# Kernel optimization log

Measured on AMD Instinct MI355X. Metric: run time of the kernel, lower is better.

The kernel has to match this reference:

```python
import jax, jax.numpy as jnp
import numpy as np
from jax import lax

K = 3
STRIDE = 1
PAD = 1
DIL = 1


def setup_inputs() -> dict:
    key = jax.random.key(0)
    k1, k2, k3 = jax.random.split(key, 3)
    B, C, H, W = 8, 128, 64, 64
    O = 128
    x = jax.random.normal(k1, (B, C, H, W), jnp.float32)
    # offset-predicting conv weights (small init -> small offsets, as in DCN practice)
    w_off = jax.random.normal(k2, (2 * K * K, C, K, K), jnp.float32) * 0.01
    b_off = jnp.zeros((2 * K * K,), jnp.float32)
    # deformable conv weight [O, Cin, K, K], bias=False in the source
    w = jax.random.normal(k3, (O, C, K, K), jnp.float32) * (1.0 / np.sqrt(C * K * K))
    return {"x": x, "w_off": w_off, "b_off": b_off, "w": w}


def _deform_conv(x, offset, w):
    # x: [B,C,H,W]; offset: [B, 2*K*K, Ho, Wo]; w: [O,C,K,K]
    B, C, H, W = x.shape
    Ho, Wo = offset.shape[2], offset.shape[3]
    K2 = K * K
    off = offset.reshape(B, K2, 2, Ho, Wo)
    oy, ox = off[:, :, 0], off[:, :, 1]            # [B,K2,Ho,Wo]
    ky = (jnp.arange(K2) // K).astype(jnp.float32)  # kernel row per tap
    kx = (jnp.arange(K2) % K).astype(jnp.float32)
    base_y = (jnp.arange(Ho) * STRIDE - PAD).astype(jnp.float32)
    base_x = (jnp.arange(Wo) * STRIDE - PAD).astype(jnp.float32)
    py = base_y[None, None, :, None] + ky[None, :, None, None] * DIL + oy
    px = base_x[None, None, None, :] + kx[None, :, None, None] * DIL + ox

    y0 = jnp.floor(py)
    x0 = jnp.floor(px)
    dy = py - y0
    dx = px - x0
    y0i = y0.astype(jnp.int32)
    x0i = x0.astype(jnp.int32)
    bidx = jnp.arange(B)[:, None, None, None]

    def gather(yi, xi):
        valid = (yi >= 0) & (yi < H) & (xi >= 0) & (xi < W)
        yc = jnp.clip(yi, 0, H - 1)
        xc = jnp.clip(xi, 0, W - 1)
        v = x[bidx, :, yc, xc]  # [B,K2,Ho,Wo,C]
        return v * valid[..., None]

    v00 = gather(y0i, x0i)
    v01 = gather(y0i, x0i + 1)
    v10 = gather(y0i + 1, x0i)
    v11 = gather(y0i + 1, x0i + 1)
    samp = (v00 * ((1 - dy) * (1 - dx))[..., None]
            + v01 * ((1 - dy) * dx)[..., None]
            + v10 * (dy * (1 - dx))[..., None]
            + v11 * (dy * dx)[..., None])  # [B,K2,Ho,Wo,C]

    O = w.shape[0]
    return jnp.einsum('bkhwc,ock->bohw', samp, w.reshape(O, C, K2))


def reference(x, w_off, b_off, w):
    # offset conv: standard conv2d, stride/pad/dilation as in __init__
    offset = lax.conv_general_dilated(
        x, w_off, window_strides=(STRIDE, STRIDE),
        padding=[(PAD, PAD), (PAD, PAD)], rhs_dilation=(DIL, DIL))
    offset = offset + b_off[None, :, None, None]
    return _deform_conv(x, offset, w)
```

## Files before the change

### kernel.cpp

```cpp
#include <hip/hip_runtime.h>

#define B_ 8
#define C_ 128
#define H_ 64
#define W_ 64
#define O_ 128
#define F_ 18
#define K2_ 9
#define HW_ 4096
#define CK2_ 1152

typedef __attribute__((ext_vector_type(8))) short short8_t;
typedef __attribute__((ext_vector_type(4))) float f32x4_t;

__device__ inline short bf16r(float f) {
  unsigned u = __builtin_bit_cast(unsigned, f);
  u += 0x7FFFu + ((u >> 16) & 1u);
  return (short)(u >> 16);
}
__device__ inline float bf2f(short s) {
  unsigned u = ((unsigned)(unsigned short)s) << 16;
  return __builtin_bit_cast(float, u);
}

__global__ __launch_bounds__(256) void prep_all_kernel(
    const float* __restrict__ w, const float* __restrict__ w_off,
    const float* __restrict__ x,
    short* __restrict__ w_bt2, short* __restrict__ w_ot2,
    short* __restrict__ x_t) {
  __shared__ float tile[128][65];
  int bid = blockIdx.x, t = threadIdx.x;
  if (bid < 576) {
    int i = bid * 256 + t;
    int kk2 = i & 31, o = (i >> 5) & 127, ks = i >> 12;
    w_bt2[i] = bf16r(w[(o * C_ + (ks & 3) * 32 + kk2) * K2_ + (ks >> 2)]);
  } else if (bid < 720) {
    int i = (bid - 576) * 256 + t;
    int kk2 = i & 31, f = (i >> 5) & 31, ks = i >> 10;
    w_ot2[i] = (f < F_) ? bf16r(w_off[(f * C_ + (ks & 3) * 32 + kk2) * K2_ + (ks >> 2)])
                        : (short)0;
  } else {
    int xb_id = bid - 720;
    int b = xb_id >> 6;
    int p_base = (xb_id & 63) << 6;
    const float* xb = x + ((long)b << 19);
#pragma unroll
    for (int i = 0; i < 32; ++i) {
      int idx = (i << 8) + t;
      int c = idx >> 6, p = idx & 63;
      tile[c][p] = xb[((long)c << 12) + p_base + p];
    }
    __syncthreads();
#pragma unroll
    for (int i = 0; i < 32; ++i) {
      int idx = (i << 8) + t;
      int p = idx >> 7, c = idx & 127;
      x_t[(((long)(b << 12) + p_base + p) << 7) + c] = bf16r(tile[c][p]);
    }
  }
}

__device__ inline short8_t lds16(const short* xs, int pix, int ch) {
  return *(const short8_t*)(xs + (pix << 7) + ((ch ^ (pix & 7)) << 3));
}

__global__ __launch_bounds__(512, 2) void fused_deform_kernel(
    const short* __restrict__ x_t, const short* __restrict__ w_ot2,
    const float* __restrict__ b_off, const short* __restrict__ w_bt2,
    float* __restrict__ out) {
  __shared__ short xs[8 * 64 * 128];

  int tid = threadIdx.x;
  int wv = tid >> 6, lane = tid & 63;
  int fr = lane & 15, q = lane >> 4;
  int bid = (int)blockIdx.x;
  int b = bid & 7;
  int strip = bid >> 3;
  int ho0 = strip << 1;
  int ys = max(ho0 - 3, 0), ye = min(ho0 + 4, H_ - 1);

  const short* xtb = x_t + ((long)b << 19);

#pragma unroll
  for (int i = 0; i < 16; ++i) {
    int ci = (i << 9) + tid;
    int pix = ci >> 4, ch = ci & 15;
    int y = ys + (pix >> 6);
    if (y <= ye) {
      short8_t v = *(const short8_t*)(xtb + (((y << 6) + (pix & 63)) << 7) + (ch << 3));
      *(short8_t*)(xs + (pix << 7) + ((ch ^ (pix & 7)) << 3)) = v;
    }
  }
  __syncthreads();

  int pos_l = (wv << 4) + fr;
  int row_l = pos_l >> 6;
  int wo = pos_l & 63;
  int ho = ho0 + row_l;

  f32x4_t oacc0 = (f32x4_t){0.f, 0.f, 0.f, 0.f};
  f32x4_t oacc1 = (f32x4_t){0.f, 0.f, 0.f, 0.f};
#pragma unroll
  for (int kt = 0; kt < 9; ++kt) {
    int y = ho + kt / 3 - 1, xx = wo + kt % 3 - 1;
    bool ok = (y >= 0) & (y < H_) & (xx >= 0) & (xx < W_);
    int yc = min(max(y, 0), H_ - 1), xc = min(max(xx, 0), W_ - 1);
    int pixA = ((yc - ys) << 6) + xc;
#pragma unroll
    for (int s = 0; s < 4; ++s) {
      short8_t bfv = lds16(xs, pixA, (s << 2) + q);
      if (!ok) bfv = (short8_t){0, 0, 0, 0, 0, 0, 0, 0};
      int ks = (kt << 2) + s;
      short8_t a0 = *(const short8_t*)(w_ot2 + (((ks << 5) + fr) << 5) + (q << 3));
      short8_t a1 = *(const short8_t*)(w_ot2 + (((ks << 5) + 16 + fr) << 5) + (q << 3));
      oacc0 = __builtin_amdgcn_mfma_f32_16x16x32_bf16(a0, bfv, oacc0, 0, 0, 0);
      oacc1 = __builtin_amdgcn_mfma_f32_16x16x32_bf16(a1, bfv, oacc1, 0, 0, 0);
    }
  }

  f32x4_t acc[8];
#pragma unroll
  for (int nf = 0; nf < 8; ++nf) acc[nf] = (f32x4_t){0.f, 0.f, 0.f, 0.f};

#pragma unroll
  for (int kt = 0; kt < 9; ++kt) {
    float oy, ox;
    if (kt < 8) {
      oy = __shfl(oacc0[(2 * kt) & 3], fr + ((kt >> 1) << 4), 64);
      ox = __shfl(oacc0[(2 * kt + 1) & 3], fr + ((kt >> 1) << 4), 64);
    } else {
      oy = __shfl(oacc1[0], fr, 64);
      ox = __shfl(oacc1[1], fr, 64);
    }
    oy += b_off[2 * kt];
    ox += b_off[2 * kt + 1];

    float py = (float)(ho + kt / 3 - 1) + oy;
    float px = (float)(wo + kt % 3 - 1) + ox;
    float fy0 = floorf(py), fx0 = floorf(px);
    float dy = py - fy0, dx = px - fx0;
    int y0 = (int)fy0, x0 = (int)fx0;
    int y1 = y0 + 1, x1 = x0 + 1;
    float my0 = (y0 >= 0 && y0 < H_) ? 1.f : 0.f;
    float my1 = (y1 >= 0 && y1 < H_) ? 1.f : 0.f;
    float mx0 = (x0 >= 0 && x0 < W_) ? 1.f : 0.f;
    float mx1 = (x1 >= 0 && x1 < W_) ? 1.f : 0.f;
    float w00 = (1.f - dy) * (1.f - dx) * my0 * mx0;
    float w01 = (1.f - dy) * dx * my0 * mx1;
    float w10 = dy * (1.f - dx) * my1 * mx0;
    float w11 = dy * dx * my1 * mx1;
    int y0c = min(max(y0, 0), H_ - 1), y1c = min(max(y1, 0), H_ - 1);
    int x0c = min(max(x0, 0), W_ - 1), x1c = min(max(x1, 0), W_ - 1);
    int p00 = ((y0c - ys) << 6) + x0c, p01 = ((y0c - ys) << 6) + x1c;
    int p10 = ((y1c - ys) << 6) + x0c, p11 = ((y1c - ys) << 6) + x1c;

    short8_t v00[4], v01[4], v10[4], v11[4];
    unsigned long long bad = __ballot((y0c < ys) || (y1c > ye));
    if (bad == 0ULL) {
#pragma unroll
      for (int s = 0; s < 4; ++s) {
        int ch = (s << 2) + q;
        v00[s] = lds16(xs, p00, ch);
        v01[s] = lds16(xs, p01, ch);
        v10[s] = lds16(xs, p10, ch);
        v11[s] = lds16(xs, p11, ch);
      }
    } else {
      const short* g00 = xtb + (((y0c << 6) + x0c) << 7);
      const short* g01 = xtb + (((y0c << 6) + x1c) << 7);
      const short* g10 = xtb + (((y1c << 6) + x0c) << 7);
      const short* g11 = xtb + (((y1c << 6) + x1c) << 7);
#pragma unroll
      for (int s = 0; s < 4; ++s) {
        int c0 = (s << 5) + (q << 3);
        v00[s] = *(const short8_t*)(g00 + c0);
        v01[s] = *(const short8_t*)(g01 + c0);
        v10[s] = *(const short8_t*)(g10 + c0);
        v11[s] = *(const short8_t*)(g11 + c0);
      }
    }

#pragma unroll
    for (int s = 0; s < 4; ++s) {
      short8_t sf;
#pragma unroll
      for (int j = 0; j < 8; ++j) {
        float v = w00 * bf2f(v00[s][j]) + w01 * bf2f(v01[s][j]) +
                  w10 * bf2f(v10[s][j]) + w11 * bf2f(v11[s][j]);
        sf[j] = bf16r(v);
      }
      int ks = (kt << 2) + s;
      const short* wp = w_bt2 + (((ks << 7) + fr) << 5) + (q << 3);
#pragma unroll
      for (int nf = 0; nf < 8; ++nf) {
        short8_t wf = *(const short8_t*)(wp + (nf << 9));
        acc[nf] = __builtin_amdgcn_mfma_f32_16x16x32_bf16(wf, sf, acc[nf], 0, 0, 0);
      }
    }
  }

  float* ob = out + ((long)(b * O_) << 12) + (ho << 6) + wo;
#pragma unroll
  for (int nf = 0; nf < 8; ++nf) {
#pragma unroll
    for (int r = 0; r < 4; ++r) {
      ob[(long)(((nf << 4) + (q << 2) + r)) << 12] = acc[nf][r];
    }
  }
}

extern "C" void kernel_launch(void* const* d_in, const int* in_sizes, int n_in,
                              void* d_out, int out_size, void* d_ws, size_t ws_size,
                              hipStream_t stream) {
  const float* x     = (const float*)d_in[0];
  const float* w_off = (const float*)d_in[1];
  const float* b_off = (const float*)d_in[2];
  const float* w     = (const float*)d_in[3];
  float* out = (float*)d_out;

  short* w_bt2 = (short*)d_ws;
  short* w_ot2 = (short*)((char*)d_ws + 294912);
  short* x_t   = (short*)((char*)d_ws + 294912 + 73728);

  prep_all_kernel<<<1232, 256, 0, stream>>>(w, w_off, x, w_bt2, w_ot2, x_t);
  fused_deform_kernel<<<256, 512, 0, stream>>>(x_t, w_ot2, b_off, w_bt2, out);
}
```

Before: 61.90 us.

## Use 2D 8x16 output tiles with smaller LDS halo and packed bf16 conversion

Changes each block's work from a two-row full-width strip to an 8x16 2D tile. This shrinks the staged LDS halo window to 14x22 pixels, which allows four blocks per CU instead of two. It also replaces the per-element bf16 unpack and round with 32-bit lo/hi extraction and the hardware v_cvt_pk_bf16_f32 instruction. The extra x-direction halo bound check may send more waves to the global-memory fallback path, and the bf16 rounding now depends on the hardware converter rather than the software round.

```diff
diff --git a/kernel.cpp b/kernel.cpp
--- a/kernel.cpp
+++ b/kernel.cpp
@@ -10,17 +10,23 @@
 #define HW_ 4096
 #define CK2_ 1152
 
+#define WR_ 14
+#define WC_ 22
+
 typedef __attribute__((ext_vector_type(8))) short short8_t;
 typedef __attribute__((ext_vector_type(4))) float f32x4_t;
+typedef __attribute__((ext_vector_type(4))) unsigned int uint4_t;
 
 __device__ inline short bf16r(float f) {
   unsigned u = __builtin_bit_cast(unsigned, f);
   u += 0x7FFFu + ((u >> 16) & 1u);
   return (short)(u >> 16);
 }
-__device__ inline float bf2f(short s) {
-  unsigned u = ((unsigned)(unsigned short)s) << 16;
-  return __builtin_bit_cast(float, u);
+__device__ inline float bflo(unsigned u) {
+  return __builtin_bit_cast(float, u << 16);
+}
+__device__ inline float bfhi(unsigned u) {
+  return __builtin_bit_cast(float, u & 0xFFFF0000u);
 }
 
 __global__ __launch_bounds__(256) void prep_all_kernel(
@@ -64,39 +70,40 @@
   return *(const short8_t*)(xs + (pix << 7) + ((ch ^ (pix & 7)) << 3));
 }
 
-__global__ __launch_bounds__(512, 2) void fused_deform_kernel(
+__global__ __launch_bounds__(512, 4) void fused_deform_kernel(
     const short* __restrict__ x_t, const short* __restrict__ w_ot2,
     const float* __restrict__ b_off, const short* __restrict__ w_bt2,
     float* __restrict__ out) {
-  __shared__ short xs[8 * 64 * 128];
+  __shared__ short xs[WR_ * WC_ * 128];
 
   int tid = threadIdx.x;
   int wv = tid >> 6, lane = tid & 63;
   int fr = lane & 15, q = lane >> 4;
   int bid = (int)blockIdx.x;
   int b = bid & 7;
-  int strip = bid >> 3;
-  int ho0 = strip << 1;
-  int ys = max(ho0 - 3, 0), ye = min(ho0 + 4, H_ - 1);
+  int tile_id = bid >> 3;
+  int ho0 = (tile_id >> 2) << 3;
+  int x0b = (tile_id & 3) << 4;
+  int ys  = min(max(ho0 - 3, 0), H_ - WR_);
+  int xsL = min(max(x0b - 3, 0), W_ - WC_);
+  int ye2 = ys + WR_ - 1, xe2 = xsL + WC_ - 1;
 
   const short* xtb = x_t + ((long)b << 19);
 
 #pragma unroll
-  for (int i = 0; i < 16; ++i) {
+  for (int i = 0; i < 10; ++i) {
     int ci = (i << 9) + tid;
-    int pix = ci >> 4, ch = ci & 15;
-    int y = ys + (pix >> 6);
-    if (y <= ye) {
-      short8_t v = *(const short8_t*)(xtb + (((y << 6) + (pix & 63)) << 7) + (ch << 3));
+    if (ci < WR_ * WC_ * 16) {
+      int pix = ci >> 4, ch = ci & 15;
+      int yr = pix / WC_, xr = pix - yr * WC_;
+      short8_t v = *(const short8_t*)(xtb + ((((ys + yr) << 6) + xsL + xr) << 7) + (ch << 3));
       *(short8_t*)(xs + (pix << 7) + ((ch ^ (pix & 7)) << 3)) = v;
     }
   }
   __syncthreads();
 
-  int pos_l = (wv << 4) + fr;
-  int row_l = pos_l >> 6;
-  int wo = pos_l & 63;
-  int ho = ho0 + row_l;
+  int ho = ho0 + wv;
+  int wo = x0b + fr;
 
   f32x4_t oacc0 = (f32x4_t){0.f, 0.f, 0.f, 0.f};
   f32x4_t oacc1 = (f32x4_t){0.f, 0.f, 0.f, 0.f};
@@ -105,7 +112,7 @@
     int y = ho + kt / 3 - 1, xx = wo + kt % 3 - 1;
     bool ok = (y >= 0) & (y < H_) & (xx >= 0) & (xx < W_);
     int yc = min(max(y, 0), H_ - 1), xc = min(max(xx, 0), W_ - 1);
-    int pixA = ((yc - ys) << 6) + xc;
+    int pixA = (yc - ys) * WC_ + (xc - xsL);
 #pragma unroll
     for (int s = 0; s < 4; ++s) {
       short8_t bfv = lds16(xs, pixA, (s << 2) + q);
@@ -151,11 +158,12 @@
     float w11 = dy * dx * my1 * mx1;
     int y0c = min(max(y0, 0), H_ - 1), y1c = min(max(y1, 0), H_ - 1);
     int x0c = min(max(x0, 0), W_ - 1), x1c = min(max(x1, 0), W_ - 1);
-    int p00 = ((y0c - ys) << 6) + x0c, p01 = ((y0c - ys) << 6) + x1c;
-    int p10 = ((y1c - ys) << 6) + x0c, p11 = ((y1c - ys) << 6) + x1c;
+    int p00 = (y0c - ys) * WC_ + (x0c - xsL), p01 = p00 + (x1c - x0c);
+    int p10 = (y1c - ys) * WC_ + (x0c - xsL), p11 = p10 + (x1c - x0c);
 
     short8_t v00[4], v01[4], v10[4], v11[4];
-    unsigned long long bad = __ballot((y0c < ys) || (y1c > ye));
+    unsigned long long bad =
+        __ballot((y0c < ys) || (y1c > ye2) || (x0c < xsL) || (x1c > xe2));
     if (bad == 0ULL) {
 #pragma unroll
       for (int s = 0; s < 4; ++s) {
@@ -182,13 +190,22 @@
 
 #pragma unroll
     for (int s = 0; s < 4; ++s) {
-      short8_t sf;
-#pragma unroll
-      for (int j = 0; j < 8; ++j) {
-        float v = w00 * bf2f(v00[s][j]) + w01 * bf2f(v01[s][j]) +
-                  w10 * bf2f(v10[s][j]) + w11 * bf2f(v11[s][j]);
-        sf[j] = bf16r(v);
-      }
+      uint4_t u00 = __builtin_bit_cast(uint4_t, v00[s]);
+      uint4_t u01 = __builtin_bit_cast(uint4_t, v01[s]);
+      uint4_t u10 = __builtin_bit_cast(uint4_t, v10[s]);
+      uint4_t u11 = __builtin_bit_cast(uint4_t, v11[s]);
+      uint4_t sfu;
+#pragma unroll
+      for (int d = 0; d < 4; ++d) {
+        float rlo = w00 * bflo(u00[d]) + w01 * bflo(u01[d]) +
+                    w10 * bflo(u10[d]) + w11 * bflo(u11[d]);
+        float rhi = w00 * bfhi(u00[d]) + w01 * bfhi(u01[d]) +
+                    w10 * bfhi(u10[d]) + w11 * bfhi(u11[d]);
+        unsigned p;
+        asm("v_cvt_pk_bf16_f32 %0, %1, %2" : "=v"(p) : "v"(rlo), "v"(rhi));
+        sfu[d] = p;
+      }
+      short8_t sf = __builtin_bit_cast(short8_t, sfu);
       int ks = (kt << 2) + s;
       const short* wp = w_bt2 + (((ks << 7) + fr) << 5) + (q << 3);
 #pragma unroll
```

After: 69.55 us. 1.12x slower.
